# Kernel optimization log

Hardware: AMD Instinct MI355X
Metric: run time of the kernel (lower is better)

The kernel has to match this reference:

```python
import jax, jax.numpy as jnp
import numpy as np


def setup_inputs() -> dict:
    key = jax.random.key(0)
    k1, k2 = jax.random.split(key)
    B, C, H, W = 8, 256, 128, 128
    x = jax.random.normal(k1, (B, C, H, W), dtype=jnp.float32)
    # prior plays the role of torch.rand initial selection score (shape [B, H*W])
    prior = jax.random.uniform(k2, (B, H * W), dtype=jnp.float32)
    return {"x": x, "prior": prior, "nbVec": 16}


def reference(x, prior, nbVec):
    # representativeVectors(x, nbVec, prior=prior, onlySimSample=True, applyUMAP=False)
    B, C, H, W = x.shape
    N = H * W
    xf = x.transpose(0, 2, 3, 1).reshape(B, N, C)  # [B, N, C]
    batch = jnp.arange(B)
    EPS = 1e-12  # numerical guard for sqrt at the selected point (dist == 0)

    def step(carry, i):
        score, selpos = carry  # score: [B, N] selection score, selpos: [B, N]
        # i == 0: deterministic center pick; else data-dependent argmax of score
        ind = jnp.where(i == 0, N // 2, jnp.argmax(score, axis=1))  # [B]
        selpos = selpos.at[batch, ind].add(1.0)
        rv = xf[batch, ind]  # gathered representative candidates [B, C]
        # exp(-euclidean_dist / 20) similarity to every spatial position
        d = jnp.sqrt(jnp.sum((xf - rv[:, None, :]) ** 2, axis=-1) + EPS)  # [B, N]
        sim = jnp.exp(-d / 20.0)
        simNorm = sim / jnp.sum(sim, axis=1, keepdims=True)
        repr_vec = jnp.einsum('bnc,bn->bc', xf, simNorm)  # weighted reduction
        score = jnp.where(i == 0, 1.0 - sim, (1.0 - sim) * score)
        return (score, selpos), (repr_vec, sim)

    init = (prior, jnp.zeros((B, N), dtype=x.dtype))
    (_, selpos), (reprVecs, sims) = jax.lax.scan(step, init, jnp.arange(nbVec))
    # reprVecs: [nbVec, B, C]; sims -> [nbVec, B, 1, H, W]; selpos -> [B, 1, H, W]
    return reprVecs, sims.reshape(nbVec, B, 1, H, W), selpos.reshape(B, 1, H, W)
```

## Files before the change

### kernel.cpp

```cpp
#include <hip/hip_runtime.h>
#include <math.h>

#define BB 8
#define CC 256
#define HH 128
#define WW 128
#define NN (HH*WW)
#define NBVEC 16
#define CSPLIT 16
#define CCHUNK (CC/CSPLIT)
#define NBX (NN/256)


__global__ __launch_bounds__(256, 8)
void fused_kernel(const float* __restrict__ x,
                  float* __restrict__ out,
                  const double* __restrict__ bmaxv,
                  const int* __restrict__ bmaxi,
                  float* __restrict__ d2part,
                  double* __restrict__ wpart, int iter)
{
    const int b  = blockIdx.z;
    const int cz = blockIdx.y;
    const int nb = blockIdx.x;
    const int t  = threadIdx.x;
    const int n  = nb*256 + t;

    __shared__ float s_x[CCHUNK][257];
    __shared__ float s_sim[256];
    __shared__ float s_rv[CCHUNK];
    __shared__ union UScratch {
        double part[16][CCHUNK];
        struct { double val[NBX]; int idx[NBX]; } mx;
    } s_u;

    float* out_sims   = out + (size_t)NBVEC*BB*CC;
    float* out_selpos = out_sims + (size_t)NBVEC*BB*NN;

    int sel = NN/2;
    if (iter > 0 && iter < NBVEC) {
        if (t < NBX) { s_u.mx.val[t] = bmaxv[b*NBX + t]; s_u.mx.idx[t] = bmaxi[b*NBX + t]; }
        __syncthreads();
        for (int s = NBX/2; s > 0; s >>= 1) {
            if (t < s) {
                double v2 = s_u.mx.val[t+s]; int i2 = s_u.mx.idx[t+s];
                if (v2 > s_u.mx.val[t] || (v2 == s_u.mx.val[t] && i2 < s_u.mx.idx[t])) {
                    s_u.mx.val[t] = v2; s_u.mx.idx[t] = i2;
                }
            }
            __syncthreads();
        }
        sel = s_u.mx.idx[0];
    }

    if (iter < NBVEC) {
        if (t < CCHUNK)
            s_rv[t] = x[((size_t)b*CC + (size_t)cz*CCHUNK + t)*NN + sel];
        if (t == 0 && nb == 0 && cz == 0)
            out_selpos[(size_t)b*NN + sel] += 1.0f;
    }
    if (iter > 0)
        s_sim[t] = out_sims[(size_t)(iter-1)*BB*NN + (size_t)b*NN + n];
    __syncthreads();

    const float* xb = x + ((size_t)b*CC + (size_t)cz*CCHUNK)*NN;
    float r[CCHUNK];
    #pragma unroll
    for (int c = 0; c < CCHUNK; ++c)
        r[c] = xb[(size_t)c*NN + n];
    if (iter > 0) {
        #pragma unroll
        for (int c = 0; c < CCHUNK; ++c)
            s_x[c][t] = r[c];
    }

    if (iter < NBVEC) {
        double acc = 0.0;
        #pragma unroll
        for (int c = 0; c < CCHUNK; ++c) {
            double diff = (double)r[c] - (double)s_rv[c];
            acc = fma(diff, diff, acc);
        }
        d2part[((size_t)cz*BB + b)*NN + n] = (float)acc;
    }
    __syncthreads();

    if (iter > 0) {
        const int c = t & 15;
        const int g = t >> 4;
        double w = 0.0;
        #pragma unroll
        for (int k = 0; k < 16; ++k) {
            const int nn2 = g*16 + k;
            w = fma((double)s_sim[nn2], (double)s_x[c][nn2], w);
        }
        s_u.part[g][c] = w;
        __syncthreads();
        if (t < CCHUNK) {
            double t0 = 0.0, t1 = 0.0;
            #pragma unroll
            for (int gg = 0; gg < 16; gg += 2) {
                t0 += s_u.part[gg][t];
                t1 += s_u.part[gg+1][t];
            }
            wpart[((size_t)nb*BB + b)*CC + (size_t)cz*CCHUNK + t] = t0 + t1;
        }
    }
}

__global__ void finish_kernel(float* __restrict__ out,
                              double* __restrict__ score,
                              const float* __restrict__ d2part,
                              double* __restrict__ sumSim,
                              const double* __restrict__ wpart,
                              double* __restrict__ bmaxv,
                              int* __restrict__ bmaxi, int iter)
{
    const int b = blockIdx.y;
    const int t = threadIdx.x;
    const int n = blockIdx.x * 256 + t;
    const size_t si = (size_t)b*NN + n;
    const int lane = t & 63;
    const int wave = t >> 6;

    double a0 = 0.0, a1 = 0.0;
    #pragma unroll
    for (int cz = 0; cz < CSPLIT; cz += 2) {
        a0 += (double)d2part[((size_t)cz*BB + b)*NN + n];
        a1 += (double)d2part[((size_t)(cz+1)*BB + b)*NN + n];
    }
    double d2 = a0 + a1;

    double d   = sqrt(d2 + 1e-12);
    double sim = exp(-(d / 20.0));

    float* out_sims = out + (size_t)NBVEC*BB*CC;
    out_sims[(size_t)iter*BB*NN + si] = (float)sim;

    double sc;
    if (iter == 0) sc = 1.0 - sim;
    else           sc = (1.0 - sim) * score[si];
    score[si] = sc;

    double v = sim;
    #pragma unroll
    for (int off = 32; off > 0; off >>= 1) v += __shfl_down(v, off, 64);

    double bv = sc; int bi = n;
    #pragma unroll
    for (int off = 32; off > 0; off >>= 1) {
        double ov = __shfl_down(bv, off, 64);
        int    oi = __shfl_down(bi, off, 64);
        if (ov > bv || (ov == bv && oi < bi)) { bv = ov; bi = oi; }
    }

    __shared__ double s_ws[4];
    __shared__ double s_wv[4];
    __shared__ int    s_wi[4];
    if (lane == 0) { s_ws[wave] = v; s_wv[wave] = bv; s_wi[wave] = bi; }
    __syncthreads();
    if (t == 0) {
        double tot = ((s_ws[0] + s_ws[1]) + (s_ws[2] + s_ws[3]));
        atomicAdd(&sumSim[(size_t)(iter & 1)*BB + b], tot);
        double cv = s_wv[0]; int ci = s_wi[0];
        #pragma unroll
        for (int w = 1; w < 4; ++w) {
            if (s_wv[w] > cv || (s_wv[w] == cv && s_wi[w] < ci)) { cv = s_wv[w]; ci = s_wi[w]; }
        }
        bmaxv[(size_t)b*NBX + blockIdx.x] = cv;
        bmaxi[(size_t)b*NBX + blockIdx.x] = ci;
    }

    if (iter > 0 && blockIdx.x == 0) {
        const int slotPrev = (iter-1) & 1;
        double ss = sumSim[(size_t)slotPrev*BB + b];
        if (t < CC) {
            double c0 = 0.0, c1 = 0.0, c2 = 0.0, c3 = 0.0;
            for (int nb = 0; nb < NBX; nb += 4) {
                c0 += wpart[((size_t)(nb+0)*BB + b)*CC + t];
                c1 += wpart[((size_t)(nb+1)*BB + b)*CC + t];
                c2 += wpart[((size_t)(nb+2)*BB + b)*CC + t];
                c3 += wpart[((size_t)(nb+3)*BB + b)*CC + t];
            }
            double tot = ((c0 + c1) + (c2 + c3));
            out[(size_t)(iter-1)*BB*CC + (size_t)b*CC + t] = (float)(tot / ss);
        }
        __syncthreads();
        if (t == 0) sumSim[(size_t)slotPrev*BB + b] = 0.0;
    }
}

__global__ void final_repr_kernel(float* __restrict__ out,
                                  const double* __restrict__ sumSim,
                                  const double* __restrict__ wpart)
{
    const int b = blockIdx.x;
    const int t = threadIdx.x;
    double ss = sumSim[(size_t)((NBVEC-1) & 1)*BB + b];
    if (t < CC) {
        double c0 = 0.0, c1 = 0.0, c2 = 0.0, c3 = 0.0;
        for (int nb = 0; nb < NBX; nb += 4) {
            c0 += wpart[((size_t)(nb+0)*BB + b)*CC + t];
            c1 += wpart[((size_t)(nb+1)*BB + b)*CC + t];
            c2 += wpart[((size_t)(nb+2)*BB + b)*CC + t];
            c3 += wpart[((size_t)(nb+3)*BB + b)*CC + t];
        }
        double tot = ((c0 + c1) + (c2 + c3));
        out[(size_t)(NBVEC-1)*BB*CC + (size_t)b*CC + t] = (float)(tot / ss);
    }
}

extern "C" void kernel_launch(void* const* d_in, const int* in_sizes, int n_in,
                              void* d_out, int out_size, void* d_ws, size_t ws_size,
                              hipStream_t stream)
{
    const float* x = (const float*)d_in[0];
    float* out = (float*)d_out;

    char* ws = (char*)d_ws;
    double* score  = (double*)(ws);
    float*  d2part = (float*) (ws + 1048576);
    double* wpart  = (double*)(ws + 9437184);
    double* sumSim = (double*)(ws + 10485760);
    double* bmaxv  = (double*)(ws + 10485888);
    int*    bmaxi  = (int*)   (ws + 10489984);

    float* out_selpos = out + (size_t)NBVEC*BB*CC + (size_t)NBVEC*BB*NN;
    hipMemsetAsync(out_selpos, 0, (size_t)BB*NN*sizeof(float), stream);
    hipMemsetAsync(sumSim, 0, 2*BB*sizeof(double), stream);

    for (int i = 0; i <= NBVEC; ++i) {
        fused_kernel<<<dim3(NBX, CSPLIT, BB), 256, 0, stream>>>(
            x, out, bmaxv, bmaxi, d2part, wpart, i);
        if (i < NBVEC)
            finish_kernel<<<dim3(NBX, BB), 256, 0, stream>>>(
                out, score, d2part, sumSim, wpart, bmaxv, bmaxi, i);
    }
    final_repr_kernel<<<BB, 256, 0, stream>>>(out, sumSim, wpart);
}
```

Measured before the change: 861.4 us.

## Move argmax reduction and rv gather into finish kernel via last-block ticket

The per-block redundant argmax reduction over block maxima and the strided gather of the selected vector are moved out of every fused_kernel block. Instead, the last finishing block per batch (found with an atomic ticket and threadfence) reduces the maxima, gathers the selected rv into a workspace buffer and updates selpos. The fused kernel also now loads x with float4 row-wise coalesced loads into shared memory instead of per-thread strided scalar loads. This adds a ticket memset, an init kernel and a serialized last-block tail in finish_kernel.

```diff
diff --git a/kernel.cpp b/kernel.cpp
--- a/kernel.cpp
+++ b/kernel.cpp
@@ -15,8 +15,7 @@
 __global__ __launch_bounds__(256, 8)
 void fused_kernel(const float* __restrict__ x,
                   float* __restrict__ out,
-                  const double* __restrict__ bmaxv,
-                  const int* __restrict__ bmaxi,
+                  const float* __restrict__ rv,
                   float* __restrict__ d2part,
                   double* __restrict__ wpart, int iter)
 {
@@ -24,66 +23,45 @@
     const int cz = blockIdx.y;
     const int nb = blockIdx.x;
     const int t  = threadIdx.x;
-    const int n  = nb*256 + t;
-
-    __shared__ float s_x[CCHUNK][257];
-    __shared__ float s_sim[256];
-    __shared__ float s_rv[CCHUNK];
-    __shared__ union UScratch {
-        double part[16][CCHUNK];
-        struct { double val[NBX]; int idx[NBX]; } mx;
-    } s_u;
-
-    float* out_sims   = out + (size_t)NBVEC*BB*CC;
-    float* out_selpos = out_sims + (size_t)NBVEC*BB*NN;
-
-    int sel = NN/2;
-    if (iter > 0 && iter < NBVEC) {
-        if (t < NBX) { s_u.mx.val[t] = bmaxv[b*NBX + t]; s_u.mx.idx[t] = bmaxi[b*NBX + t]; }
-        __syncthreads();
-        for (int s = NBX/2; s > 0; s >>= 1) {
-            if (t < s) {
-                double v2 = s_u.mx.val[t+s]; int i2 = s_u.mx.idx[t+s];
-                if (v2 > s_u.mx.val[t] || (v2 == s_u.mx.val[t] && i2 < s_u.mx.idx[t])) {
-                    s_u.mx.val[t] = v2; s_u.mx.idx[t] = i2;
-                }
-            }
-            __syncthreads();
-        }
-        sel = s_u.mx.idx[0];
-    }
-
-    if (iter < NBVEC) {
-        if (t < CCHUNK)
-            s_rv[t] = x[((size_t)b*CC + (size_t)cz*CCHUNK + t)*NN + sel];
-        if (t == 0 && nb == 0 && cz == 0)
-            out_selpos[(size_t)b*NN + sel] += 1.0f;
-    }
+
+    __shared__ float  s_x[CCHUNK][257];
+    __shared__ float  s_sim[256];
+    __shared__ float  s_rv[CCHUNK];
+    __shared__ double s_part[16][CCHUNK];
+
+    const float* out_sims = out + (size_t)NBVEC*BB*CC;
+
+    if (iter < NBVEC && t < CCHUNK)
+        s_rv[t] = rv[(size_t)b*CC + (size_t)cz*CCHUNK + t];
     if (iter > 0)
-        s_sim[t] = out_sims[(size_t)(iter-1)*BB*NN + (size_t)b*NN + n];
+        s_sim[t] = out_sims[(size_t)(iter-1)*BB*NN + (size_t)b*NN + nb*256 + t];
+
+    const int row = t >> 4;
+    const int l16 = t & 15;
+    const float* xrow = x + ((size_t)b*CC + (size_t)cz*CCHUNK + row)*NN + (size_t)nb*256;
+    float4 v0 = *(const float4*)(xrow + l16*4);
+    float4 v1 = *(const float4*)(xrow + l16*4 + 64);
+    float4 v2 = *(const float4*)(xrow + l16*4 + 128);
+    float4 v3 = *(const float4*)(xrow + l16*4 + 192);
+    s_x[row][l16*4+0]       = v0.x; s_x[row][l16*4+1]       = v0.y;
+    s_x[row][l16*4+2]       = v0.z; s_x[row][l16*4+3]       = v0.w;
+    s_x[row][l16*4+64]      = v1.x; s_x[row][l16*4+65]      = v1.y;
+    s_x[row][l16*4+66]      = v1.z; s_x[row][l16*4+67]      = v1.w;
+    s_x[row][l16*4+128]     = v2.x; s_x[row][l16*4+129]     = v2.y;
+    s_x[row][l16*4+130]     = v2.z; s_x[row][l16*4+131]     = v2.w;
+    s_x[row][l16*4+192]     = v3.x; s_x[row][l16*4+193]     = v3.y;
+    s_x[row][l16*4+194]     = v3.z; s_x[row][l16*4+195]     = v3.w;
     __syncthreads();
-
-    const float* xb = x + ((size_t)b*CC + (size_t)cz*CCHUNK)*NN;
-    float r[CCHUNK];
-    #pragma unroll
-    for (int c = 0; c < CCHUNK; ++c)
-        r[c] = xb[(size_t)c*NN + n];
-    if (iter > 0) {
-        #pragma unroll
-        for (int c = 0; c < CCHUNK; ++c)
-            s_x[c][t] = r[c];
-    }
 
     if (iter < NBVEC) {
         double acc = 0.0;
         #pragma unroll
         for (int c = 0; c < CCHUNK; ++c) {
-            double diff = (double)r[c] - (double)s_rv[c];
+            double diff = (double)s_x[c][t] - (double)s_rv[c];
             acc = fma(diff, diff, acc);
         }
-        d2part[((size_t)cz*BB + b)*NN + n] = (float)acc;
-    }
-    __syncthreads();
+        d2part[((size_t)cz*BB + b)*NN + (size_t)nb*256 + t] = (float)acc;
+    }
 
     if (iter > 0) {
         const int c = t & 15;
@@ -94,27 +72,30 @@
             const int nn2 = g*16 + k;
             w = fma((double)s_sim[nn2], (double)s_x[c][nn2], w);
         }
-        s_u.part[g][c] = w;
+        s_part[g][c] = w;
         __syncthreads();
         if (t < CCHUNK) {
             double t0 = 0.0, t1 = 0.0;
             #pragma unroll
             for (int gg = 0; gg < 16; gg += 2) {
-                t0 += s_u.part[gg][t];
-                t1 += s_u.part[gg+1][t];
+                t0 += s_part[gg][t];
+                t1 += s_part[gg+1][t];
             }
             wpart[((size_t)nb*BB + b)*CC + (size_t)cz*CCHUNK + t] = t0 + t1;
         }
     }
 }
 
-__global__ void finish_kernel(float* __restrict__ out,
+__global__ void finish_kernel(const float* __restrict__ x,
+                              float* __restrict__ out,
                               double* __restrict__ score,
                               const float* __restrict__ d2part,
                               double* __restrict__ sumSim,
                               const double* __restrict__ wpart,
                               double* __restrict__ bmaxv,
-                              int* __restrict__ bmaxi, int iter)
+                              int* __restrict__ bmaxi,
+                              float* __restrict__ rv,
+                              int* __restrict__ ticket, int iter)
 {
     const int b = blockIdx.y;
     const int t = threadIdx.x;
@@ -123,6 +104,16 @@
     const int lane = t & 63;
     const int wave = t >> 6;
 
+    __shared__ double s_ws[4];
+    __shared__ double s_wv[4];
+    __shared__ int    s_wi[4];
+    __shared__ int    s_last;
+    __shared__ double s_val[NBX];
+    __shared__ int    s_idx[NBX];
+
+    float* out_sims   = out + (size_t)NBVEC*BB*CC;
+    float* out_selpos = out_sims + (size_t)NBVEC*BB*NN;
+
     double a0 = 0.0, a1 = 0.0;
     #pragma unroll
     for (int cz = 0; cz < CSPLIT; cz += 2) {
@@ -134,7 +125,6 @@
     double d   = sqrt(d2 + 1e-12);
     double sim = exp(-(d / 20.0));
 
-    float* out_sims = out + (size_t)NBVEC*BB*CC;
     out_sims[(size_t)iter*BB*NN + si] = (float)sim;
 
     double sc;
@@ -154,9 +144,6 @@
         if (ov > bv || (ov == bv && oi < bi)) { bv = ov; bi = oi; }
     }
 
-    __shared__ double s_ws[4];
-    __shared__ double s_wv[4];
-    __shared__ int    s_wi[4];
     if (lane == 0) { s_ws[wave] = v; s_wv[wave] = bv; s_wi[wave] = bi; }
     __syncthreads();
     if (t == 0) {
@@ -182,11 +169,51 @@
                 c2 += wpart[((size_t)(nb+2)*BB + b)*CC + t];
                 c3 += wpart[((size_t)(nb+3)*BB + b)*CC + t];
             }
-            double tot = ((c0 + c1) + (c2 + c3));
-            out[(size_t)(iter-1)*BB*CC + (size_t)b*CC + t] = (float)(tot / ss);
+            double tot2 = ((c0 + c1) + (c2 + c3));
+            out[(size_t)(iter-1)*BB*CC + (size_t)b*CC + t] = (float)(tot2 / ss);
         }
         __syncthreads();
         if (t == 0) sumSim[(size_t)slotPrev*BB + b] = 0.0;
+    }
+
+    if (iter < NBVEC-1) {
+        if (t == 0) {
+            __threadfence();
+            int old = atomicAdd(&ticket[iter*BB + b], 1);
+            s_last = (old == NBX-1) ? 1 : 0;
+        }
+        __syncthreads();
+        if (s_last) {
+            __threadfence();
+            if (t < NBX) { s_val[t] = bmaxv[(size_t)b*NBX + t];
+                           s_idx[t] = bmaxi[(size_t)b*NBX + t]; }
+            __syncthreads();
+            for (int s = NBX/2; s > 0; s >>= 1) {
+                if (t < s) {
+                    double v2 = s_val[t+s]; int i2 = s_idx[t+s];
+                    if (v2 > s_val[t] || (v2 == s_val[t] && i2 < s_idx[t])) {
+                        s_val[t] = v2; s_idx[t] = i2;
+                    }
+                }
+                __syncthreads();
+            }
+            const int sel = s_idx[0];
+            rv[(size_t)b*CC + t] = x[((size_t)b*CC + t)*NN + sel];
+            if (t == 0) out_selpos[(size_t)b*NN + sel] += 1.0f;
+        }
+    }
+}
+
+__global__ void init_rv_kernel(const float* __restrict__ x,
+                               float* __restrict__ out,
+                               float* __restrict__ rv)
+{
+    const int b = blockIdx.x;
+    const int t = threadIdx.x;
+    rv[(size_t)b*CC + t] = x[((size_t)b*CC + t)*NN + NN/2];
+    if (t == 0) {
+        float* out_selpos = out + (size_t)NBVEC*BB*CC + (size_t)NBVEC*BB*NN;
+        out_selpos[(size_t)b*NN + NN/2] += 1.0f;
     }
 }
 
@@ -224,17 +251,22 @@
     double* sumSim = (double*)(ws + 10485760);
     double* bmaxv  = (double*)(ws + 10485888);
     int*    bmaxi  = (int*)   (ws + 10489984);
+    float*  rv     = (float*) (ws + 10492032);
+    int*    ticket = (int*)   (ws + 10500224);
 
     float* out_selpos = out + (size_t)NBVEC*BB*CC + (size_t)NBVEC*BB*NN;
     hipMemsetAsync(out_selpos, 0, (size_t)BB*NN*sizeof(float), stream);
     hipMemsetAsync(sumSim, 0, 2*BB*sizeof(double), stream);
+    hipMemsetAsync(ticket, 0, NBVEC*BB*sizeof(int), stream);
+
+    init_rv_kernel<<<BB, 256, 0, stream>>>(x, out, rv);
 
     for (int i = 0; i <= NBVEC; ++i) {
         fused_kernel<<<dim3(NBX, CSPLIT, BB), 256, 0, stream>>>(
-            x, out, bmaxv, bmaxi, d2part, wpart, i);
+            x, out, rv, d2part, wpart, i);
         if (i < NBVEC)
             finish_kernel<<<dim3(NBX, BB), 256, 0, stream>>>(
-                out, score, d2part, sumSim, wpart, bmaxv, bmaxi, i);
+                x, out, score, d2part, sumSim, wpart, bmaxv, bmaxi, rv, ticket, i);
     }
     final_repr_kernel<<<BB, 256, 0, stream>>>(out, sumSim, wpart);
 }
```

New measurement: 1.006 ms. 16.8% more time.

## Process four spatial sub-tiles per block with register prefetch of next tile

Applied to the files above, without the earlier changes.

Each fused_kernel block now walks four 256-position sub-tiles instead of one, so the grid shrinks fourfold. The x and previous-sim values for the next sub-tile are loaded into registers while the current one is computed from shared memory, overlapping global loads with compute. The argmax reduction and rv gather are now amortised over more positions per block. In exchange there is less block-level parallelism, 2048 blocks instead of 8192, and extra syncthreads per sub-tile. The d2 computation now reads x from shared memory rather than registers.

```diff
diff --git a/kernel.cpp b/kernel.cpp
--- a/kernel.cpp
+++ b/kernel.cpp
@@ -10,6 +10,8 @@
 #define CSPLIT 16
 #define CCHUNK (CC/CSPLIT)
 #define NBX (NN/256)
+#define NBB 16
+#define NSUB 4
 
 
 __global__ __launch_bounds__(256, 8)
@@ -24,7 +26,6 @@
     const int cz = blockIdx.y;
     const int nb = blockIdx.x;
     const int t  = threadIdx.x;
-    const int n  = nb*256 + t;
 
     __shared__ float s_x[CCHUNK][257];
     __shared__ float s_sim[256];
@@ -37,6 +38,15 @@
     float* out_sims   = out + (size_t)NBVEC*BB*CC;
     float* out_selpos = out_sims + (size_t)NBVEC*BB*NN;
 
+    const float* xb   = x + ((size_t)b*CC + (size_t)cz*CCHUNK)*NN + (size_t)nb*(NSUB*256);
+    const float* simb = out_sims + (size_t)(iter-1)*BB*NN + (size_t)b*NN + (size_t)nb*(NSUB*256);
+    float r[CCHUNK];
+    #pragma unroll
+    for (int c = 0; c < CCHUNK; ++c)
+        r[c] = xb[(size_t)c*NN + t];
+    float simreg = 0.0f;
+    if (iter > 0) simreg = simb[t];
+
     int sel = NN/2;
     if (iter > 0 && iter < NBVEC) {
         if (t < NBX) { s_u.mx.val[t] = bmaxv[b*NBX + t]; s_u.mx.idx[t] = bmaxi[b*NBX + t]; }
@@ -59,51 +69,56 @@
         if (t == 0 && nb == 0 && cz == 0)
             out_selpos[(size_t)b*NN + sel] += 1.0f;
     }
-    if (iter > 0)
-        s_sim[t] = out_sims[(size_t)(iter-1)*BB*NN + (size_t)b*NN + n];
-    __syncthreads();
-
-    const float* xb = x + ((size_t)b*CC + (size_t)cz*CCHUNK)*NN;
-    float r[CCHUNK];
-    #pragma unroll
-    for (int c = 0; c < CCHUNK; ++c)
-        r[c] = xb[(size_t)c*NN + n];
-    if (iter > 0) {
+
+    for (int sub = 0; sub < NSUB; ++sub) {
+        __syncthreads();
         #pragma unroll
         for (int c = 0; c < CCHUNK; ++c)
             s_x[c][t] = r[c];
-    }
-
-    if (iter < NBVEC) {
-        double acc = 0.0;
-        #pragma unroll
-        for (int c = 0; c < CCHUNK; ++c) {
-            double diff = (double)r[c] - (double)s_rv[c];
-            acc = fma(diff, diff, acc);
-        }
-        d2part[((size_t)cz*BB + b)*NN + n] = (float)acc;
-    }
-    __syncthreads();
-
-    if (iter > 0) {
-        const int c = t & 15;
-        const int g = t >> 4;
-        double w = 0.0;
-        #pragma unroll
-        for (int k = 0; k < 16; ++k) {
-            const int nn2 = g*16 + k;
-            w = fma((double)s_sim[nn2], (double)s_x[c][nn2], w);
-        }
-        s_u.part[g][c] = w;
-        __syncthreads();
-        if (t < CCHUNK) {
-            double t0 = 0.0, t1 = 0.0;
+        if (iter > 0) s_sim[t] = simreg;
+        __syncthreads();
+
+        if (sub + 1 < NSUB) {
+            const int off = (sub+1)*256;
             #pragma unroll
-            for (int gg = 0; gg < 16; gg += 2) {
-                t0 += s_u.part[gg][t];
-                t1 += s_u.part[gg+1][t];
-            }
-            wpart[((size_t)nb*BB + b)*CC + (size_t)cz*CCHUNK + t] = t0 + t1;
+            for (int c = 0; c < CCHUNK; ++c)
+                r[c] = xb[(size_t)c*NN + off + t];
+            if (iter > 0) simreg = simb[off + t];
+        }
+
+        const int n = nb*(NSUB*256) + sub*256 + t;
+
+        if (iter < NBVEC) {
+            double acc = 0.0;
+            #pragma unroll
+            for (int c = 0; c < CCHUNK; ++c) {
+                double diff = (double)s_x[c][t] - (double)s_rv[c];
+                acc = fma(diff, diff, acc);
+            }
+            d2part[((size_t)cz*BB + b)*NN + n] = (float)acc;
+        }
+
+        if (iter > 0) {
+            const int c = t & 15;
+            const int g = t >> 4;
+            double w = 0.0;
+            #pragma unroll
+            for (int k = 0; k < 16; ++k) {
+                const int nn2 = g*16 + k;
+                w = fma((double)s_sim[nn2], (double)s_x[c][nn2], w);
+            }
+            s_u.part[g][c] = w;
+            __syncthreads();
+            if (t < CCHUNK) {
+                double t0 = 0.0, t1 = 0.0;
+                #pragma unroll
+                for (int gg = 0; gg < 16; gg += 2) {
+                    t0 += s_u.part[gg][t];
+                    t1 += s_u.part[gg+1][t];
+                }
+                const int nbg = nb*NSUB + sub;
+                wpart[((size_t)nbg*BB + b)*CC + (size_t)cz*CCHUNK + t] = t0 + t1;
+            }
         }
     }
 }
@@ -182,8 +197,8 @@
                 c2 += wpart[((size_t)(nb+2)*BB + b)*CC + t];
                 c3 += wpart[((size_t)(nb+3)*BB + b)*CC + t];
             }
-            double tot = ((c0 + c1) + (c2 + c3));
-            out[(size_t)(iter-1)*BB*CC + (size_t)b*CC + t] = (float)(tot / ss);
+            double tot2 = ((c0 + c1) + (c2 + c3));
+            out[(size_t)(iter-1)*BB*CC + (size_t)b*CC + t] = (float)(tot2 / ss);
         }
         __syncthreads();
         if (t == 0) sumSim[(size_t)slotPrev*BB + b] = 0.0;
@@ -230,7 +245,7 @@
     hipMemsetAsync(sumSim, 0, 2*BB*sizeof(double), stream);
 
     for (int i = 0; i <= NBVEC; ++i) {
-        fused_kernel<<<dim3(NBX, CSPLIT, BB), 256, 0, stream>>>(
+        fused_kernel<<<dim3(NBB, CSPLIT, BB), 256, 0, stream>>>(
             x, out, bmaxv, bmaxi, d2part, wpart, i);
         if (i < NBVEC)
             finish_kernel<<<dim3(NBX, BB), 256, 0, stream>>>(
```

New measurement: 840.9 us. 2.4% less time.
